# Kernel optimization log

Hardware: AMD Instinct MI355X
Metric: run time of the kernel (lower is better)

Reference implementation:

```python
import jax, jax.numpy as jnp
import numpy as np

N = 100000      # nodes
E = 1000000     # edges per relation
D_IN = 128
D_OUT = 128
SLOPE = 0.2
N_REL = 3


def setup_inputs() -> dict:
    key = jax.random.key(0)
    ks = jax.random.split(key, 1 + 4 * N_REL)
    inp = {"H": jax.random.normal(ks[0], (N, D_IN), dtype=jnp.float32)}
    xav_w = float(np.sqrt(6.0 / (D_IN + D_OUT)))   # xavier_uniform bound for W
    xav_a = float(np.sqrt(6.0 / (1 + 2 * D_OUT)))  # xavier_uniform on a viewed as [1, 2d]
    for i in range(N_REL):
        inp[f"row_{i}"] = jax.random.randint(ks[1 + 4 * i], (E,), 0, N, dtype=jnp.int64)
        inp[f"col_{i}"] = jax.random.randint(ks[2 + 4 * i], (E,), 0, N, dtype=jnp.int64)
        inp[f"W_{i}"] = jax.random.uniform(ks[3 + 4 * i], (D_IN, D_OUT), jnp.float32, -xav_w, xav_w)
        inp[f"a_{i}"] = jax.random.uniform(ks[4 + 4 * i], (2 * D_OUT,), jnp.float32, -xav_a, xav_a)
    inp["bias"] = jnp.zeros((D_OUT,), jnp.float32)
    return inp


def _relation_agg(H, W, a, row, col):
    # 1) transform: Wh = H @ W_r  [N, d]
    Wh = H @ W
    d = Wh.shape[1]
    # 2) edge scores: e_ij = leaky_relu(a[:d].Wh[row] + a[d:].Wh[col])
    s_dst = Wh @ a[:d]   # coefficient for destination (row) side  [N]
    s_src = Wh @ a[d:]   # coefficient for source (col) side       [N]
    e = jax.nn.leaky_relu(s_dst[row] + s_src[col], negative_slope=SLOPE)  # [E]
    # 3) segment softmax over incoming edges of each destination node
    e_max = jax.ops.segment_max(e, row, num_segments=N)          # [N]
    e_shift = jnp.exp(e - e_max[row])                            # [E]
    e_sum = jax.ops.segment_sum(e_shift, row, num_segments=N)    # [N]
    alpha = e_shift / jnp.maximum(e_sum[row], 1e-12)             # [E]
    # 4) weighted aggregation of source features
    return jax.ops.segment_sum(alpha[:, None] * Wh[col], row, num_segments=N)  # [N, d]


def reference(H, row_0, col_0, row_1, col_1, row_2, col_2,
              W_0, W_1, W_2, a_0, a_1, a_2, bias):
    rows = (row_0, row_1, row_2)
    cols = (col_0, col_1, col_2)
    Ws = (W_0, W_1, W_2)
    As = (a_0, a_1, a_2)
    agg = jnp.zeros((N, D_OUT), H.dtype)
    for r in range(N_REL):
        agg = agg + _relation_agg(H, Ws[r], As[r], rows[r], cols[r])
    return agg + bias
```

## Files before the change

### kernel.cpp

```cpp
#include <hip/hip_runtime.h>

#define SLOPE 0.2f

typedef unsigned int uint;
typedef unsigned short ushort;
typedef __attribute__((ext_vector_type(8))) short short8;
typedef __attribute__((ext_vector_type(4))) float f32x4;

#define BINW 2048
#define BINSHIFT 11

__device__ inline ushort f2bf(float f) {
    uint u = __float_as_uint(f);
    uint r = (u + 0x7FFFu + ((u >> 16) & 1u)) >> 16;
    return (ushort)r;
}
__device__ inline uint pack2bf(float lo, float hi) {
    return (uint)f2bf(lo) | ((uint)f2bf(hi) << 16);
}
__device__ inline float bfl(uint u) { return __uint_as_float(u << 16); }
__device__ inline float bfh(uint u) { return __uint_as_float(u & 0xFFFF0000u); }

__global__ void wt3(const float* __restrict__ W0, const float* __restrict__ W1,
                    const float* __restrict__ W2, ushort* __restrict__ WT) {
    int r = blockIdx.x;
    const float* W = (r == 0) ? W0 : (r == 1) ? W1 : W2;
    ushort* wt = WT + r * 16384;
    for (int i = threadIdx.x; i < 16384; i += 256) {
        int k = i >> 7, n = i & 127;
        wt[n * 128 + k] = f2bf(W[i]);
    }
}

__global__ __launch_bounds__(256) void gemm3(const float* __restrict__ H,
                                             const ushort* __restrict__ WT,
                                             ushort* __restrict__ Wh0,
                                             ushort* __restrict__ Wh1,
                                             ushort* __restrict__ Wh2, int N) {
    __shared__ ushort lds[16384];
    const int brow = blockIdx.x * 128;
    const int t = threadIdx.x;

    for (int c = t; c < 2048; c += 256) {
        int r = c >> 4;
        int kb = (c & 15) << 4;
        int gr = brow + r;
        uint4 u = make_uint4(0, 0, 0, 0);
        if (gr < N) {
            const float* hp = H + (size_t)gr * 128 + (kb >> 1);
            float4 v0 = *reinterpret_cast<const float4*>(hp);
            float4 v1 = *reinterpret_cast<const float4*>(hp + 4);
            u.x = pack2bf(v0.x, v0.y);
            u.y = pack2bf(v0.z, v0.w);
            u.z = pack2bf(v1.x, v1.y);
            u.w = pack2bf(v1.z, v1.w);
        }
        int dst = (r << 8) + (kb ^ ((r & 7) << 4));
        *reinterpret_cast<uint4*>((char*)lds + dst) = u;
    }
    __syncthreads();

    const int wave = t >> 6, lane = t & 63;
    const int l16 = lane & 15, lhi = lane >> 4;

    for (int rel = 0; rel < 3; ++rel) {
        ushort* Wh = (rel == 0) ? Wh0 : (rel == 1) ? Wh1 : Wh2;
        const ushort* wt = WT + rel * 16384;

        short8 bf[2][4];
#pragma unroll
        for (int nt = 0; nt < 2; ++nt) {
            int n = wave * 32 + nt * 16 + l16;
#pragma unroll
            for (int ks = 0; ks < 4; ++ks)
                bf[nt][ks] = *reinterpret_cast<const short8*>(wt + n * 128 + ks * 32 + lhi * 8);
        }

        f32x4 acc[8][2];
#pragma unroll
        for (int mt = 0; mt < 8; ++mt) { acc[mt][0] = (f32x4)(0.f); acc[mt][1] = (f32x4)(0.f); }

#pragma unroll
        for (int ks = 0; ks < 4; ++ks) {
#pragma unroll
            for (int mt = 0; mt < 8; ++mt) {
                int r = mt * 16 + l16;
                int kb = (ks * 32 + lhi * 8) * 2;
                int addr = (r << 8) + (kb ^ ((r & 7) << 4));
                short8 af = *reinterpret_cast<const short8*>((char*)lds + addr);
                acc[mt][0] = __builtin_amdgcn_mfma_f32_16x16x32_bf16(af, bf[0][ks], acc[mt][0], 0, 0, 0);
                acc[mt][1] = __builtin_amdgcn_mfma_f32_16x16x32_bf16(af, bf[1][ks], acc[mt][1], 0, 0, 0);
            }
        }

#pragma unroll
        for (int mt = 0; mt < 8; ++mt)
#pragma unroll
            for (int nt = 0; nt < 2; ++nt)
#pragma unroll
                for (int reg = 0; reg < 4; ++reg) {
                    int gr = brow + mt * 16 + lhi * 4 + reg;
                    if (gr < N)
                        Wh[(size_t)gr * 128 + wave * 32 + nt * 16 + l16] = f2bf(acc[mt][nt][reg]);
                }
    }
}

__global__ __launch_bounds__(256) void scores_k(const uint* __restrict__ wh0,
                                                const uint* __restrict__ wh1,
                                                const uint* __restrict__ wh2,
                                                const float* __restrict__ a0,
                                                const float* __restrict__ a1,
                                                const float* __restrict__ a2,
                                                float* __restrict__ sd,
                                                float* __restrict__ ss, int N) {
    int node = blockIdx.x * 16 + (threadIdx.x >> 4);
    int ql = threadIdx.x & 15;
    if (node >= N) return;
#pragma unroll
    for (int r = 0; r < 3; ++r) {
        const uint* wh = (r == 0) ? wh0 : (r == 1) ? wh1 : wh2;
        const float* a = (r == 0) ? a0 : (r == 1) ? a1 : a2;
        const uint4 v = reinterpret_cast<const uint4*>(wh + ((size_t)node << 6))[ql];
        float f0 = bfl(v.x), f1 = bfh(v.x), f2 = bfl(v.y), f3 = bfh(v.y);
        float f4 = bfl(v.z), f5 = bfh(v.z), f6 = bfl(v.w), f7 = bfh(v.w);
        float4 aL0 = *reinterpret_cast<const float4*>(a + ql * 8);
        float4 aL1 = *reinterpret_cast<const float4*>(a + ql * 8 + 4);
        float4 aR0 = *reinterpret_cast<const float4*>(a + 128 + ql * 8);
        float4 aR1 = *reinterpret_cast<const float4*>(a + 128 + ql * 8 + 4);
        float pd = f0 * aL0.x + f1 * aL0.y + f2 * aL0.z + f3 * aL0.w +
                   f4 * aL1.x + f5 * aL1.y + f6 * aL1.z + f7 * aL1.w;
        float ps = f0 * aR0.x + f1 * aR0.y + f2 * aR0.z + f3 * aR0.w +
                   f4 * aR1.x + f5 * aR1.y + f6 * aR1.z + f7 * aR1.w;
#pragma unroll
        for (int off = 1; off < 16; off <<= 1) {
            pd += __shfl_xor(pd, off);
            ps += __shfl_xor(ps, off);
        }
        if (ql == 0) { sd[r * N + node] = pd; ss[r * N + node] = ps; }
    }
}

__global__ __launch_bounds__(256) void binhist(const int* __restrict__ r0,
                                               const int* __restrict__ r1,
                                               const int* __restrict__ r2,
                                               int* __restrict__ bincnt, int E, int N, int nbins) {
    __shared__ int h[256];
    int t = threadIdx.x;
    h[t] = 0;
    __syncthreads();
    int base = blockIdx.x * 4096;
#pragma unroll
    for (int k = 0; k < 16; ++k) {
        int i = base + k * 256 + t;
        if (i < 3 * E) {
            int r = (i >= 2 * E) ? 2 : (i >= E) ? 1 : 0;
            int li = i - r * E;
            const int* rp = (r == 0) ? r0 : (r == 1) ? r1 : r2;
            int idx = r * N + __builtin_nontemporal_load(rp + li);
            atomicAdd(&h[idx >> BINSHIFT], 1);
        }
    }
    __syncthreads();
    if (t < nbins && h[t]) atomicAdd(&bincnt[t], h[t]);
}

__global__ __launch_bounds__(256) void binscan(const int* __restrict__ bincnt,
                                               int* __restrict__ binbase,
                                               int* __restrict__ gbincur, int nbins, int total) {
    __shared__ int sA[256], sB[256];
    int t = threadIdx.x;
    int v = (t < nbins) ? bincnt[t] : 0;
    sA[t] = v;
    __syncthreads();
    int* pa = sA; int* pb = sB;
    for (int off = 1; off < 256; off <<= 1) {
        int x = pa[t] + ((t >= off) ? pa[t - off] : 0);
        pb[t] = x;
        __syncthreads();
        int* tmp = pa; pa = pb; pb = tmp;
    }
    if (t < nbins) {
        int excl = pa[t] - v;
        binbase[t] = excl;
        gbincur[t] = excl;
    }
    if (t == 0) binbase[nbins] = total;
}

__global__ __launch_bounds__(256) void binscatter(const int* __restrict__ r0, const int* __restrict__ r1,
                                                  const int* __restrict__ r2, const int* __restrict__ c0,
                                                  const int* __restrict__ c1, const int* __restrict__ c2,
                                                  const float* __restrict__ sd, const float* __restrict__ ss,
                                                  int* __restrict__ gbincur, uint2* __restrict__ binned,
                                                  int E, int N, int nbins) {
    __shared__ uint2 staged[4096];
    __shared__ int hist[256], sB[256], curi[256], gbase[256];
    const int t = threadIdx.x;
    hist[t] = 0;
    __syncthreads();

    uint2 rec[16];
    short bn[16];
    const int base = blockIdx.x * 4096;
#pragma unroll
    for (int k = 0; k < 16; ++k) {
        int i = base + k * 256 + t;
        bn[k] = -1;
        if (i < 3 * E) {
            int r = (i >= 2 * E) ? 2 : (i >= E) ? 1 : 0;
            int li = i - r * E;
            const int* rp = (r == 0) ? r0 : (r == 1) ? r1 : r2;
            const int* cp = (r == 0) ? c0 : (r == 1) ? c1 : c2;
            int rr = __builtin_nontemporal_load(rp + li);
            int cc = __builtin_nontemporal_load(cp + li);
            int idx = r * N + rr;
            int b = idx >> BINSHIFT;
            uint lo = (uint)(idx & (BINW - 1));
            float x = sd[idx] + ss[r * N + cc];
            x = (x > 0.f) ? x : SLOPE * x;
            float w = __expf(x);
            rec[k] = make_uint2((uint)cc | (lo << 17), __float_as_uint(w));
            bn[k] = (short)b;
            atomicAdd(&hist[b], 1);
        }
    }
    __syncthreads();

    int v = hist[t];
    int* pa = hist; int* pb = sB;
    for (int off = 1; off < 256; off <<= 1) {
        int x = pa[t] + ((t >= off) ? pa[t - off] : 0);
        pb[t] = x;
        __syncthreads();
        int* tmp = pa; pa = pb; pb = tmp;
    }
    sB[t] = pa[t] - v;
    curi[t] = pa[t] - v;
    if (t < nbins && v > 0) gbase[t] = atomicAdd(&gbincur[t], v);
    __syncthreads();

#pragma unroll
    for (int k = 0; k < 16; ++k)
        if (bn[k] >= 0) {
            int p = atomicAdd(&curi[bn[k]], 1);
            staged[p] = rec[k];
        }
    __syncthreads();

    const int wave = t >> 6, lane = t & 63;
    for (int b = wave; b < nbins; b += 4) {
        int s = sB[b];
        int len = hist[b] - s;
        if (len <= 0) continue;
        int g = gbase[b];
        for (int j = lane; j < len; j += 64) binned[g + j] = staged[s + j];
    }
}

__global__ __launch_bounds__(256) void binsort(const uint2* __restrict__ binned,
                                               const int* __restrict__ binbase,
                                               uint2* __restrict__ wc, int* __restrict__ offs, int L) {
    __shared__ int s1[BINW];
    __shared__ int wsum[4];
    const int b = blockIdx.x, t = threadIdx.x;
    const int start = binbase[b], end = binbase[b + 1];
    const int ibase = b << BINSHIFT;
    const int width = min(BINW, L - ibase);

    for (int i = t; i < BINW; i += 256) s1[i] = 0;
    __syncthreads();
    for (int j = start + t; j < end; j += 256)
        atomicAdd(&s1[(binned[j].x >> 17) & (BINW - 1)], 1);
    __syncthreads();

    const int cb = t * 8;
    int v[8];
    int run = 0;
#pragma unroll
    for (int k = 0; k < 8; ++k) { run += s1[cb + k]; v[k] = run; }
    const int lane = t & 63, wv = t >> 6;
    int x = run;
#pragma unroll
    for (int off = 1; off < 64; off <<= 1) {
        int y = __shfl_up(x, off);
        if (lane >= off) x += y;
    }
    if (lane == 63) wsum[wv] = x;
    __syncthreads();
    int pre = x - run;
#pragma unroll
    for (int w = 0; w < 3; ++w) if (wv > w) pre += wsum[w];

#pragma unroll
    for (int k = 0; k < 8; ++k) {
        int i = cb + k;
        if (i < width) offs[ibase + i] = start + pre + v[k];
    }
#pragma unroll
    for (int k = 0; k < 8; ++k)
        s1[cb + k] = start + pre + (k ? v[k - 1] : 0);
    __syncthreads();

    for (int j = start + t; j < end; j += 256) {
        uint2 r = binned[j];
        uint lo = (r.x >> 17) & (BINW - 1);
        int p = atomicAdd(&s1[lo], 1);
        wc[p] = make_uint2(r.y, r.x & 0x1FFFFu);
    }
}

__global__ __launch_bounds__(256) void aggregate3(const uint* __restrict__ wh0,
                                                  const uint* __restrict__ wh1,
                                                  const uint* __restrict__ wh2,
                                                  const uint2* __restrict__ wc,
                                                  const int* __restrict__ offs,
                                                  const float* __restrict__ bias,
                                                  float* __restrict__ out, int N) {
    int node = blockIdx.x * 16 + (threadIdx.x >> 4);
    int ql = threadIdx.x & 15;
    if (node >= N) return;

    float t0 = 0.f, t1 = 0.f, t2 = 0.f, t3 = 0.f, t4 = 0.f, t5 = 0.f, t6 = 0.f, t7 = 0.f;

#pragma unroll
    for (int r = 0; r < 3; ++r) {
        const uint* wh = (r == 0) ? wh0 : (r == 1) ? wh1 : wh2;
        int idx = r * N + node;
        int end = offs[idx];
        int beg = (idx == 0) ? 0 : offs[idx - 1];
        if (beg >= end) continue;

        float wsA = 0.f, wsB = 0.f;
        float a0 = 0.f, a1 = 0.f, a2 = 0.f, a3 = 0.f, a4 = 0.f, a5 = 0.f, a6 = 0.f, a7 = 0.f;
        float g0 = 0.f, g1 = 0.f, g2 = 0.f, g3 = 0.f, g4 = 0.f, g5 = 0.f, g6 = 0.f, g7 = 0.f;

        int j = beg;
        for (; j + 4 <= end; j += 4) {
            uint2 e0 = wc[j], e1 = wc[j + 1], e2 = wc[j + 2], e3 = wc[j + 3];
            uint4 v0 = reinterpret_cast<const uint4*>(wh + ((size_t)e0.y << 6))[ql];
            uint4 v1 = reinterpret_cast<const uint4*>(wh + ((size_t)e1.y << 6))[ql];
            uint4 v2 = reinterpret_cast<const uint4*>(wh + ((size_t)e2.y << 6))[ql];
            uint4 v3 = reinterpret_cast<const uint4*>(wh + ((size_t)e3.y << 6))[ql];
            float w0 = __uint_as_float(e0.x), w1 = __uint_as_float(e1.x);
            float w2 = __uint_as_float(e2.x), w3 = __uint_as_float(e3.x);
            wsA += w0 + w2;
            wsB += w1 + w3;
            a0 = fmaf(w0, bfl(v0.x), a0); a1 = fmaf(w0, bfh(v0.x), a1);
            a2 = fmaf(w0, bfl(v0.y), a2); a3 = fmaf(w0, bfh(v0.y), a3);
            a4 = fmaf(w0, bfl(v0.z), a4); a5 = fmaf(w0, bfh(v0.z), a5);
            a6 = fmaf(w0, bfl(v0.w), a6); a7 = fmaf(w0, bfh(v0.w), a7);
            g0 = fmaf(w1, bfl(v1.x), g0); g1 = fmaf(w1, bfh(v1.x), g1);
            g2 = fmaf(w1, bfl(v1.y), g2); g3 = fmaf(w1, bfh(v1.y), g3);
            g4 = fmaf(w1, bfl(v1.z), g4); g5 = fmaf(w1, bfh(v1.z), g5);
            g6 = fmaf(w1, bfl(v1.w), g6); g7 = fmaf(w1, bfh(v1.w), g7);
            a0 = fmaf(w2, bfl(v2.x), a0); a1 = fmaf(w2, bfh(v2.x), a1);
            a2 = fmaf(w2, bfl(v2.y), a2); a3 = fmaf(w2, bfh(v2.y), a3);
            a4 = fmaf(w2, bfl(v2.z), a4); a5 = fmaf(w2, bfh(v2.z), a5);
            a6 = fmaf(w2, bfl(v2.w), a6); a7 = fmaf(w2, bfh(v2.w), a7);
            g0 = fmaf(w3, bfl(v3.x), g0); g1 = fmaf(w3, bfh(v3.x), g1);
            g2 = fmaf(w3, bfl(v3.y), g2); g3 = fmaf(w3, bfh(v3.y), g3);
            g4 = fmaf(w3, bfl(v3.z), g4); g5 = fmaf(w3, bfh(v3.z), g5);
            g6 = fmaf(w3, bfl(v3.w), g6); g7 = fmaf(w3, bfh(v3.w), g7);
        }
        for (; j < end; ++j) {
            uint2 e = wc[j];
            float w = __uint_as_float(e.x);
            uint4 v = reinterpret_cast<const uint4*>(wh + ((size_t)e.y << 6))[ql];
            wsA += w;
            a0 = fmaf(w, bfl(v.x), a0); a1 = fmaf(w, bfh(v.x), a1);
            a2 = fmaf(w, bfl(v.y), a2); a3 = fmaf(w, bfh(v.y), a3);
            a4 = fmaf(w, bfl(v.z), a4); a5 = fmaf(w, bfh(v.z), a5);
            a6 = fmaf(w, bfl(v.w), a6); a7 = fmaf(w, bfh(v.w), a7);
        }
        float inv = 1.f / fmaxf(wsA + wsB, 1e-12f);
        t0 = fmaf(a0 + g0, inv, t0); t1 = fmaf(a1 + g1, inv, t1);
        t2 = fmaf(a2 + g2, inv, t2); t3 = fmaf(a3 + g3, inv, t3);
        t4 = fmaf(a4 + g4, inv, t4); t5 = fmaf(a5 + g5, inv, t5);
        t6 = fmaf(a6 + g6, inv, t6); t7 = fmaf(a7 + g7, inv, t7);
    }

    float4 b0 = *reinterpret_cast<const float4*>(bias + ql * 8);
    float4 b1 = *reinterpret_cast<const float4*>(bias + ql * 8 + 4);
    float* o = out + (size_t)node * 128 + ql * 8;
    f32x4 o0 = {t0 + b0.x, t1 + b0.y, t2 + b0.z, t3 + b0.w};
    f32x4 o1 = {t4 + b1.x, t5 + b1.y, t6 + b1.z, t7 + b1.w};
    __builtin_nontemporal_store(o0, reinterpret_cast<f32x4*>(o));
    __builtin_nontemporal_store(o1, reinterpret_cast<f32x4*>(o + 4));
}

extern "C" void kernel_launch(void* const* d_in, const int* in_sizes, int n_in,
                              void* d_out, int out_size, void* d_ws, size_t ws_size,
                              hipStream_t stream) {
    const float* H = (const float*)d_in[0];
    const int* row[3] = {(const int*)d_in[1], (const int*)d_in[5], (const int*)d_in[9]};
    const int* col[3] = {(const int*)d_in[2], (const int*)d_in[6], (const int*)d_in[10]};
    const float* W[3] = {(const float*)d_in[3], (const float*)d_in[7], (const float*)d_in[11]};
    const float* a[3] = {(const float*)d_in[4], (const float*)d_in[8], (const float*)d_in[12]};
    const float* bias = (const float*)d_in[13];

    const int N = in_sizes[0] / 128;
    const int E = in_sizes[1];
    float* out = (float*)d_out;

    const int L = 3 * N;
    const int nbins = (L + BINW - 1) >> BINSHIFT;

    char* ws = (char*)d_ws;
    size_t off = 0;
    auto alloc = [&](size_t bytes) -> void* {
        void* p = ws + off;
        off += (bytes + 255) & ~(size_t)255;
        return p;
    };

    ushort* WT = (ushort*)alloc(3 * 16384 * 2);
    ushort* Wh[3];
    for (int r = 0; r < 3; ++r) Wh[r] = (ushort*)alloc((size_t)N * 128 * 2);
    float* sd = (float*)alloc((size_t)L * 4);
    float* ss = (float*)alloc((size_t)L * 4);
    int* offs = (int*)alloc((size_t)L * 4);
    int* bincnt = (int*)alloc((size_t)(nbins + 2) * 4);
    int* binbase = (int*)alloc((size_t)(nbins + 2) * 4);
    int* gbincur = (int*)alloc((size_t)(nbins + 2) * 4);
    uint2* wc = (uint2*)alloc((size_t)3 * E * 8);
    uint2* binned = (uint2*)d_out;

    const int nbG = (N + 127) / 128;
    const int nbQ = (N + 15) / 16;
    const int nbB = (3 * E + 4095) / 4096;

    wt3<<<3, 256, 0, stream>>>(W[0], W[1], W[2], WT);
    gemm3<<<nbG, 256, 0, stream>>>(H, WT, Wh[0], Wh[1], Wh[2], N);
    scores_k<<<nbQ, 256, 0, stream>>>((const uint*)Wh[0], (const uint*)Wh[1], (const uint*)Wh[2],
                                      a[0], a[1], a[2], sd, ss, N);

    hipMemsetAsync(bincnt, 0, (size_t)(nbins + 2) * 4, stream);
    binhist<<<nbB, 256, 0, stream>>>(row[0], row[1], row[2], bincnt, E, N, nbins);
    binscan<<<1, 256, 0, stream>>>(bincnt, binbase, gbincur, nbins, 3 * E);
    binscatter<<<nbB, 256, 0, stream>>>(row[0], row[1], row[2], col[0], col[1], col[2],
                                        sd, ss, gbincur, binned, E, N, nbins);
    binsort<<<nbins, 256, 0, stream>>>(binned, binbase, wc, offs, L);

    aggregate3<<<nbQ, 256, 0, stream>>>((const uint*)Wh[0], (const uint*)Wh[1], (const uint*)Wh[2],
                                        wc, offs, bias, out, N);
}
```

Before: 319.0 us.

## Interleave relation segments per node, fold memset into wt3, deepen aggregate loads

Changes the bin index from relation-major (r*N+row) to node-major (row*3+r), so all three relation segments of a node sit next to each other in the sorted edge array and offsets. Aggregation then reads four adjacent offsets instead of three scattered pairs. The edge loop issues six gathers at once with clamped tails in place of the 4-unrolled loop plus scalar remainder. The bincnt memset is folded into the wt3 kernel, and the binscatter copy-out uses 32-lane groups. The intent is better locality and more memory-level parallelism in aggregation, at the cost of wasted masked loads on short segments and higher register pressure.

```diff
diff --git a/kernel.cpp b/kernel.cpp
--- a/kernel.cpp
+++ b/kernel.cpp
@@ -22,8 +22,10 @@
 __device__ inline float bfh(uint u) { return __uint_as_float(u & 0xFFFF0000u); }
 
 __global__ void wt3(const float* __restrict__ W0, const float* __restrict__ W1,
-                    const float* __restrict__ W2, ushort* __restrict__ WT) {
+                    const float* __restrict__ W2, ushort* __restrict__ WT,
+                    int* __restrict__ bincnt, int nbz) {
     int r = blockIdx.x;
+    if (r == 0 && threadIdx.x < nbz) bincnt[threadIdx.x] = 0;
     const float* W = (r == 0) ? W0 : (r == 1) ? W1 : W2;
     ushort* wt = WT + r * 16384;
     for (int i = threadIdx.x; i < 16384; i += 256) {
@@ -157,7 +159,7 @@
             int r = (i >= 2 * E) ? 2 : (i >= E) ? 1 : 0;
             int li = i - r * E;
             const int* rp = (r == 0) ? r0 : (r == 1) ? r1 : r2;
-            int idx = r * N + __builtin_nontemporal_load(rp + li);
+            int idx = __builtin_nontemporal_load(rp + li) * 3 + r;
             atomicAdd(&h[idx >> BINSHIFT], 1);
         }
     }
@@ -214,10 +216,10 @@
             const int* cp = (r == 0) ? c0 : (r == 1) ? c1 : c2;
             int rr = __builtin_nontemporal_load(rp + li);
             int cc = __builtin_nontemporal_load(cp + li);
-            int idx = r * N + rr;
+            int idx = rr * 3 + r;
             int b = idx >> BINSHIFT;
             uint lo = (uint)(idx & (BINW - 1));
-            float x = sd[idx] + ss[r * N + cc];
+            float x = sd[r * N + rr] + ss[r * N + cc];
             x = (x > 0.f) ? x : SLOPE * x;
             float w = __expf(x);
             rec[k] = make_uint2((uint)cc | (lo << 17), __float_as_uint(w));
@@ -248,13 +250,13 @@
         }
     __syncthreads();
 
-    const int wave = t >> 6, lane = t & 63;
-    for (int b = wave; b < nbins; b += 4) {
+    const int g32 = t >> 5, lane32 = t & 31;
+    for (int b = g32; b < nbins; b += 8) {
         int s = sB[b];
         int len = hist[b] - s;
         if (len <= 0) continue;
         int g = gbase[b];
-        for (int j = lane; j < len; j += 64) binned[g + j] = staged[s + j];
+        for (int j = lane32; j < len; j += 32) binned[g + j] = staged[s + j];
     }
 }
 
@@ -321,57 +323,54 @@
     int ql = threadIdx.x & 15;
     if (node >= N) return;
 
+    const int base = node * 3;
+    int s0 = (base == 0) ? 0 : offs[base - 1];
+    int s1 = offs[base];
+    int s2 = offs[base + 1];
+    int s3 = offs[base + 2];
+
     float t0 = 0.f, t1 = 0.f, t2 = 0.f, t3 = 0.f, t4 = 0.f, t5 = 0.f, t6 = 0.f, t7 = 0.f;
 
 #pragma unroll
     for (int r = 0; r < 3; ++r) {
-        const uint* wh = (r == 0) ? wh0 : (r == 1) ? wh1 : wh2;
-        int idx = r * N + node;
-        int end = offs[idx];
-        int beg = (idx == 0) ? 0 : offs[idx - 1];
+        const uint4* wh4 = reinterpret_cast<const uint4*>((r == 0) ? wh0 : (r == 1) ? wh1 : wh2);
+        int beg = (r == 0) ? s0 : (r == 1) ? s1 : s2;
+        int end = (r == 0) ? s1 : (r == 1) ? s2 : s3;
         if (beg >= end) continue;
 
         float wsA = 0.f, wsB = 0.f;
         float a0 = 0.f, a1 = 0.f, a2 = 0.f, a3 = 0.f, a4 = 0.f, a5 = 0.f, a6 = 0.f, a7 = 0.f;
         float g0 = 0.f, g1 = 0.f, g2 = 0.f, g3 = 0.f, g4 = 0.f, g5 = 0.f, g6 = 0.f, g7 = 0.f;
 
-        int j = beg;
-        for (; j + 4 <= end; j += 4) {
-            uint2 e0 = wc[j], e1 = wc[j + 1], e2 = wc[j + 2], e3 = wc[j + 3];
-            uint4 v0 = reinterpret_cast<const uint4*>(wh + ((size_t)e0.y << 6))[ql];
-            uint4 v1 = reinterpret_cast<const uint4*>(wh + ((size_t)e1.y << 6))[ql];
-            uint4 v2 = reinterpret_cast<const uint4*>(wh + ((size_t)e2.y << 6))[ql];
-            uint4 v3 = reinterpret_cast<const uint4*>(wh + ((size_t)e3.y << 6))[ql];
-            float w0 = __uint_as_float(e0.x), w1 = __uint_as_float(e1.x);
-            float w2 = __uint_as_float(e2.x), w3 = __uint_as_float(e3.x);
-            wsA += w0 + w2;
-            wsB += w1 + w3;
-            a0 = fmaf(w0, bfl(v0.x), a0); a1 = fmaf(w0, bfh(v0.x), a1);
-            a2 = fmaf(w0, bfl(v0.y), a2); a3 = fmaf(w0, bfh(v0.y), a3);
-            a4 = fmaf(w0, bfl(v0.z), a4); a5 = fmaf(w0, bfh(v0.z), a5);
-            a6 = fmaf(w0, bfl(v0.w), a6); a7 = fmaf(w0, bfh(v0.w), a7);
-            g0 = fmaf(w1, bfl(v1.x), g0); g1 = fmaf(w1, bfh(v1.x), g1);
-            g2 = fmaf(w1, bfl(v1.y), g2); g3 = fmaf(w1, bfh(v1.y), g3);
-            g4 = fmaf(w1, bfl(v1.z), g4); g5 = fmaf(w1, bfh(v1.z), g5);
-            g6 = fmaf(w1, bfl(v1.w), g6); g7 = fmaf(w1, bfh(v1.w), g7);
-            a0 = fmaf(w2, bfl(v2.x), a0); a1 = fmaf(w2, bfh(v2.x), a1);
-            a2 = fmaf(w2, bfl(v2.y), a2); a3 = fmaf(w2, bfh(v2.y), a3);
-            a4 = fmaf(w2, bfl(v2.z), a4); a5 = fmaf(w2, bfh(v2.z), a5);
-            a6 = fmaf(w2, bfl(v2.w), a6); a7 = fmaf(w2, bfh(v2.w), a7);
-            g0 = fmaf(w3, bfl(v3.x), g0); g1 = fmaf(w3, bfh(v3.x), g1);
-            g2 = fmaf(w3, bfl(v3.y), g2); g3 = fmaf(w3, bfh(v3.y), g3);
-            g4 = fmaf(w3, bfl(v3.z), g4); g5 = fmaf(w3, bfh(v3.z), g5);
-            g6 = fmaf(w3, bfl(v3.w), g6); g7 = fmaf(w3, bfh(v3.w), g7);
-        }
-        for (; j < end; ++j) {
-            uint2 e = wc[j];
-            float w = __uint_as_float(e.x);
-            uint4 v = reinterpret_cast<const uint4*>(wh + ((size_t)e.y << 6))[ql];
-            wsA += w;
-            a0 = fmaf(w, bfl(v.x), a0); a1 = fmaf(w, bfh(v.x), a1);
-            a2 = fmaf(w, bfl(v.y), a2); a3 = fmaf(w, bfh(v.y), a3);
-            a4 = fmaf(w, bfl(v.z), a4); a5 = fmaf(w, bfh(v.z), a5);
-            a6 = fmaf(w, bfl(v.w), a6); a7 = fmaf(w, bfh(v.w), a7);
+        for (int j = beg; j < end; j += 6) {
+            uint2 e[6];
+            uint4 v[6];
+            float w[6];
+#pragma unroll
+            for (int k = 0; k < 6; ++k) {
+                int jk = j + k;
+                jk = (jk < end) ? jk : end - 1;
+                e[k] = wc[jk];
+            }
+#pragma unroll
+            for (int k = 0; k < 6; ++k)
+                v[k] = wh4[((size_t)e[k].y << 4) + ql];
+#pragma unroll
+            for (int k = 0; k < 6; ++k)
+                w[k] = (j + k < end) ? __uint_as_float(e[k].x) : 0.f;
+#pragma unroll
+            for (int k = 0; k < 6; k += 2) {
+                wsA += w[k];
+                a0 = fmaf(w[k], bfl(v[k].x), a0); a1 = fmaf(w[k], bfh(v[k].x), a1);
+                a2 = fmaf(w[k], bfl(v[k].y), a2); a3 = fmaf(w[k], bfh(v[k].y), a3);
+                a4 = fmaf(w[k], bfl(v[k].z), a4); a5 = fmaf(w[k], bfh(v[k].z), a5);
+                a6 = fmaf(w[k], bfl(v[k].w), a6); a7 = fmaf(w[k], bfh(v[k].w), a7);
+                wsB += w[k + 1];
+                g0 = fmaf(w[k + 1], bfl(v[k + 1].x), g0); g1 = fmaf(w[k + 1], bfh(v[k + 1].x), g1);
+                g2 = fmaf(w[k + 1], bfl(v[k + 1].y), g2); g3 = fmaf(w[k + 1], bfh(v[k + 1].y), g3);
+                g4 = fmaf(w[k + 1], bfl(v[k + 1].z), g4); g5 = fmaf(w[k + 1], bfh(v[k + 1].z), g5);
+                g6 = fmaf(w[k + 1], bfl(v[k + 1].w), g6); g7 = fmaf(w[k + 1], bfh(v[k + 1].w), g7);
+            }
         }
         float inv = 1.f / fmaxf(wsA + wsB, 1e-12f);
         t0 = fmaf(a0 + g0, inv, t0); t1 = fmaf(a1 + g1, inv, t1);
@@ -430,12 +429,11 @@
     const int nbQ = (N + 15) / 16;
     const int nbB = (3 * E + 4095) / 4096;
 
-    wt3<<<3, 256, 0, stream>>>(W[0], W[1], W[2], WT);
+    wt3<<<3, 256, 0, stream>>>(W[0], W[1], W[2], WT, bincnt, nbins + 2);
     gemm3<<<nbG, 256, 0, stream>>>(H, WT, Wh[0], Wh[1], Wh[2], N);
     scores_k<<<nbQ, 256, 0, stream>>>((const uint*)Wh[0], (const uint*)Wh[1], (const uint*)Wh[2],
                                       a[0], a[1], a[2], sd, ss, N);
 
-    hipMemsetAsync(bincnt, 0, (size_t)(nbins + 2) * 4, stream);
     binhist<<<nbB, 256, 0, stream>>>(row[0], row[1], row[2], bincnt, E, N, nbins);
     binscan<<<1, 256, 0, stream>>>(bincnt, binbase, gbincur, nbins, 3 * E);
     binscatter<<<nbB, 256, 0, stream>>>(row[0], row[1], row[2], col[0], col[1], col[2],
```

New measurement: 330.4 us. 3.6% more time.

## Precompute W·a vectors, interleave relation segments per node, fuse memset

Applied to the files above, without the earlier changes.

Folds the attention vector into the weights (W·a) in the weight-transpose kernel, so scores are computed directly from H rather than from the bf16 Wh outputs. This lets the scores kernel run independently of the GEMM output. Segment indices are interleaved as node*3+r, so one node's three relation segments are adjacent and aggregate reads its offsets in one contiguous group. The bincnt memset is folded into wt3, and the binned copy-out uses 32-lane groups. Scores now come from fp32 H, which changes rounding slightly compared with scores from bf16 Wh.

```diff
diff --git a/kernel.cpp b/kernel.cpp
--- a/kernel.cpp
+++ b/kernel.cpp
@@ -22,13 +22,33 @@
 __device__ inline float bfh(uint u) { return __uint_as_float(u & 0xFFFF0000u); }
 
 __global__ void wt3(const float* __restrict__ W0, const float* __restrict__ W1,
-                    const float* __restrict__ W2, ushort* __restrict__ WT) {
+                    const float* __restrict__ W2,
+                    const float* __restrict__ a0, const float* __restrict__ a1,
+                    const float* __restrict__ a2,
+                    ushort* __restrict__ WT, float* __restrict__ wa,
+                    int* __restrict__ bincnt, int nbz) {
     int r = blockIdx.x;
+    if (r == 0 && threadIdx.x < nbz) bincnt[threadIdx.x] = 0;
     const float* W = (r == 0) ? W0 : (r == 1) ? W1 : W2;
+    const float* a = (r == 0) ? a0 : (r == 1) ? a1 : a2;
     ushort* wt = WT + r * 16384;
     for (int i = threadIdx.x; i < 16384; i += 256) {
         int k = i >> 7, n = i & 127;
         wt[n * 128 + k] = f2bf(W[i]);
+    }
+    if (threadIdx.x < 128) {
+        int k = threadIdx.x;
+        const float* wrow = W + k * 128;
+        float pd = 0.f, ps = 0.f;
+        for (int n = 0; n < 128; n += 4) {
+            float4 w4 = *reinterpret_cast<const float4*>(wrow + n);
+            float4 aL = *reinterpret_cast<const float4*>(a + n);
+            float4 aR = *reinterpret_cast<const float4*>(a + 128 + n);
+            pd += w4.x * aL.x + w4.y * aL.y + w4.z * aL.z + w4.w * aL.w;
+            ps += w4.x * aR.x + w4.y * aR.y + w4.z * aR.z + w4.w * aR.w;
+        }
+        wa[r * 256 + k] = pd;
+        wa[r * 256 + 128 + k] = ps;
     }
 }
 
@@ -106,32 +126,28 @@
     }
 }
 
-__global__ __launch_bounds__(256) void scores_k(const uint* __restrict__ wh0,
-                                                const uint* __restrict__ wh1,
-                                                const uint* __restrict__ wh2,
-                                                const float* __restrict__ a0,
-                                                const float* __restrict__ a1,
-                                                const float* __restrict__ a2,
+__global__ __launch_bounds__(256) void scores_k(const float* __restrict__ H,
+                                                const float* __restrict__ wa,
                                                 float* __restrict__ sd,
                                                 float* __restrict__ ss, int N) {
     int node = blockIdx.x * 16 + (threadIdx.x >> 4);
     int ql = threadIdx.x & 15;
     if (node >= N) return;
+    const float* hp = H + (size_t)node * 128 + ql * 8;
+    float4 h0 = *reinterpret_cast<const float4*>(hp);
+    float4 h1 = *reinterpret_cast<const float4*>(hp + 4);
 #pragma unroll
     for (int r = 0; r < 3; ++r) {
-        const uint* wh = (r == 0) ? wh0 : (r == 1) ? wh1 : wh2;
-        const float* a = (r == 0) ? a0 : (r == 1) ? a1 : a2;
-        const uint4 v = reinterpret_cast<const uint4*>(wh + ((size_t)node << 6))[ql];
-        float f0 = bfl(v.x), f1 = bfh(v.x), f2 = bfl(v.y), f3 = bfh(v.y);
-        float f4 = bfl(v.z), f5 = bfh(v.z), f6 = bfl(v.w), f7 = bfh(v.w);
-        float4 aL0 = *reinterpret_cast<const float4*>(a + ql * 8);
-        float4 aL1 = *reinterpret_cast<const float4*>(a + ql * 8 + 4);
-        float4 aR0 = *reinterpret_cast<const float4*>(a + 128 + ql * 8);
-        float4 aR1 = *reinterpret_cast<const float4*>(a + 128 + ql * 8 + 4);
-        float pd = f0 * aL0.x + f1 * aL0.y + f2 * aL0.z + f3 * aL0.w +
-                   f4 * aL1.x + f5 * aL1.y + f6 * aL1.z + f7 * aL1.w;
-        float ps = f0 * aR0.x + f1 * aR0.y + f2 * aR0.z + f3 * aR0.w +
-                   f4 * aR1.x + f5 * aR1.y + f6 * aR1.z + f7 * aR1.w;
+        const float* wd = wa + r * 256 + ql * 8;
+        const float* wsv = wa + r * 256 + 128 + ql * 8;
+        float4 d0 = *reinterpret_cast<const float4*>(wd);
+        float4 d1 = *reinterpret_cast<const float4*>(wd + 4);
+        float4 s0 = *reinterpret_cast<const float4*>(wsv);
+        float4 s1 = *reinterpret_cast<const float4*>(wsv + 4);
+        float pd = h0.x * d0.x + h0.y * d0.y + h0.z * d0.z + h0.w * d0.w +
+                   h1.x * d1.x + h1.y * d1.y + h1.z * d1.z + h1.w * d1.w;
+        float ps = h0.x * s0.x + h0.y * s0.y + h0.z * s0.z + h0.w * s0.w +
+                   h1.x * s1.x + h1.y * s1.y + h1.z * s1.z + h1.w * s1.w;
 #pragma unroll
         for (int off = 1; off < 16; off <<= 1) {
             pd += __shfl_xor(pd, off);
@@ -157,7 +173,7 @@
             int r = (i >= 2 * E) ? 2 : (i >= E) ? 1 : 0;
             int li = i - r * E;
             const int* rp = (r == 0) ? r0 : (r == 1) ? r1 : r2;
-            int idx = r * N + __builtin_nontemporal_load(rp + li);
+            int idx = __builtin_nontemporal_load(rp + li) * 3 + r;
             atomicAdd(&h[idx >> BINSHIFT], 1);
         }
     }
@@ -214,10 +230,10 @@
             const int* cp = (r == 0) ? c0 : (r == 1) ? c1 : c2;
             int rr = __builtin_nontemporal_load(rp + li);
             int cc = __builtin_nontemporal_load(cp + li);
-            int idx = r * N + rr;
+            int idx = rr * 3 + r;
             int b = idx >> BINSHIFT;
             uint lo = (uint)(idx & (BINW - 1));
-            float x = sd[idx] + ss[r * N + cc];
+            float x = sd[r * N + rr] + ss[r * N + cc];
             x = (x > 0.f) ? x : SLOPE * x;
             float w = __expf(x);
             rec[k] = make_uint2((uint)cc | (lo << 17), __float_as_uint(w));
@@ -248,13 +264,13 @@
         }
     __syncthreads();
 
-    const int wave = t >> 6, lane = t & 63;
-    for (int b = wave; b < nbins; b += 4) {
+    const int g32 = t >> 5, lane32 = t & 31;
+    for (int b = g32; b < nbins; b += 8) {
         int s = sB[b];
         int len = hist[b] - s;
         if (len <= 0) continue;
         int g = gbase[b];
-        for (int j = lane; j < len; j += 64) binned[g + j] = staged[s + j];
+        for (int j = lane32; j < len; j += 32) binned[g + j] = staged[s + j];
     }
 }
 
@@ -321,14 +337,19 @@
     int ql = threadIdx.x & 15;
     if (node >= N) return;
 
+    const int base = node * 3;
+    int s0 = (base == 0) ? 0 : offs[base - 1];
+    int s1 = offs[base];
+    int s2 = offs[base + 1];
+    int s3 = offs[base + 2];
+
     float t0 = 0.f, t1 = 0.f, t2 = 0.f, t3 = 0.f, t4 = 0.f, t5 = 0.f, t6 = 0.f, t7 = 0.f;
 
 #pragma unroll
     for (int r = 0; r < 3; ++r) {
         const uint* wh = (r == 0) ? wh0 : (r == 1) ? wh1 : wh2;
-        int idx = r * N + node;
-        int end = offs[idx];
-        int beg = (idx == 0) ? 0 : offs[idx - 1];
+        int beg = (r == 0) ? s0 : (r == 1) ? s1 : s2;
+        int end = (r == 0) ? s1 : (r == 1) ? s2 : s3;
         if (beg >= end) continue;
 
         float wsA = 0.f, wsB = 0.f;
@@ -415,6 +436,7 @@
     };
 
     ushort* WT = (ushort*)alloc(3 * 16384 * 2);
+    float* wa = (float*)alloc(3 * 256 * 4);
     ushort* Wh[3];
     for (int r = 0; r < 3; ++r) Wh[r] = (ushort*)alloc((size_t)N * 128 * 2);
     float* sd = (float*)alloc((size_t)L * 4);
@@ -430,12 +452,10 @@
     const int nbQ = (N + 15) / 16;
     const int nbB = (3 * E + 4095) / 4096;
 
-    wt3<<<3, 256, 0, stream>>>(W[0], W[1], W[2], WT);
+    wt3<<<3, 256, 0, stream>>>(W[0], W[1], W[2], a[0], a[1], a[2], WT, wa, bincnt, nbins + 2);
     gemm3<<<nbG, 256, 0, stream>>>(H, WT, Wh[0], Wh[1], Wh[2], N);
-    scores_k<<<nbQ, 256, 0, stream>>>((const uint*)Wh[0], (const uint*)Wh[1], (const uint*)Wh[2],
-                                      a[0], a[1], a[2], sd, ss, N);
-
-    hipMemsetAsync(bincnt, 0, (size_t)(nbins + 2) * 4, stream);
+    scores_k<<<nbQ, 256, 0, stream>>>(H, wa, sd, ss, N);
+
     binhist<<<nbB, 256, 0, stream>>>(row[0], row[1], row[2], bincnt, E, N, nbins);
     binscan<<<1, 256, 0, stream>>>(bincnt, binbase, gbincur, nbins, 3 * E);
     binscatter<<<nbB, 256, 0, stream>>>(row[0], row[1], row[2], col[0], col[1], col[2],
```

Measured after the change: 331.4 us. +3.9%, slower.
